# Performance work log

Measured on AMD Instinct MI355X. Metric: run time of the kernel, lower is better.

The kernel has to match this reference:

```python
import jax, jax.numpy as jnp
import numpy as np

N = 100000   # nodes
E = 1600000  # edges
NEG_SLOPE = 0.2
EPS = 1e-16


def _layer_norm(x, g, b):
    mu = jnp.mean(x, axis=-1, keepdims=True)
    var = jnp.mean((x - mu) ** 2, axis=-1, keepdims=True)
    return (x - mu) * jax.lax.rsqrt(var + 1e-5) * g + b


def _gat_layer(x, W, att_s, att_d, bias, src, dst, heads, C):
    n = x.shape[0]
    h = (x @ W.T).reshape(n, heads, C)            # [N,H,C]
    sa = jnp.sum(h * att_s, axis=-1)              # [N,H]
    da = jnp.sum(h * att_d, axis=-1)              # [N,H]
    logits = jax.nn.leaky_relu(sa[src] + da[dst], NEG_SLOPE)  # [E,H]
    m = jax.ops.segment_max(logits, dst, num_segments=n)      # [N,H]
    m = jnp.where(jnp.isfinite(m), m, 0.0)
    w = jnp.exp(logits - m[dst])                  # [E,H]
    denom = jax.ops.segment_sum(w, dst, num_segments=n)       # [N,H]
    msg = h[src] * w[:, :, None]                  # [E,H,C]
    agg = jax.ops.segment_sum(msg, dst, num_segments=n)       # [N,H,C]
    agg = agg / jnp.maximum(denom, EPS)[:, :, None]
    out = (agg + h).reshape(n, heads * C) + bias  # residual + bias
    return out


def setup_inputs() -> dict:
    key = jax.random.key(0)
    ks = jax.random.split(key, 16)
    s = 0.05
    inp = {
        "x": jax.random.normal(ks[0], (N, 128), jnp.float32),
        "edge_src": jax.random.randint(ks[1], (E,), 0, N, jnp.int32),
        "edge_dst": jax.random.randint(ks[2], (E,), 0, N, jnp.int32),
        # layer 1: in 128 -> heads=2, C=32 (out width 64)
        "W1": jax.random.normal(ks[3], (64, 128), jnp.float32) * s,
        "as1": jax.random.normal(ks[4], (2, 32), jnp.float32) * s,
        "ad1": jax.random.normal(ks[5], (2, 32), jnp.float32) * s,
        "b1": jnp.zeros((64,), jnp.float32),
        # layer 2: 64 -> heads=2, C=32
        "W2": jax.random.normal(ks[6], (64, 64), jnp.float32) * s,
        "as2": jax.random.normal(ks[7], (2, 32), jnp.float32) * s,
        "ad2": jax.random.normal(ks[8], (2, 32), jnp.float32) * s,
        "b2": jnp.zeros((64,), jnp.float32),
        # layer 3 (last): 64 -> heads=1, C=32
        "W3": jax.random.normal(ks[9], (32, 64), jnp.float32) * s,
        "as3": jax.random.normal(ks[10], (1, 32), jnp.float32) * s,
        "ad3": jax.random.normal(ks[11], (1, 32), jnp.float32) * s,
        "b3": jnp.zeros((32,), jnp.float32),
        "gamma1": jnp.ones((64,), jnp.float32),
        "beta1": jnp.zeros((64,), jnp.float32),
        "gamma2": jnp.ones((64,), jnp.float32),
        "beta2": jnp.zeros((64,), jnp.float32),
    }
    return inp


def reference(x, edge_src, edge_dst, W1, as1, ad1, b1, W2, as2, ad2, b2,
              W3, as3, ad3, b3, gamma1, beta1, gamma2, beta2):
    h = _gat_layer(x, W1, as1, ad1, b1, edge_src, edge_dst, 2, 32)
    h = jax.nn.relu(_layer_norm(h, gamma1, beta1))
    h = _gat_layer(h, W2, as2, ad2, b2, edge_src, edge_dst, 2, 32)
    h = jax.nn.relu(_layer_norm(h, gamma2, beta2))
    h = _gat_layer(h, W3, as3, ad3, b3, edge_src, edge_dst, 1, 32)
    return h
```

## Files before the change

### kernel.cpp

```cpp
#include <hip/hip_runtime.h>
#include <hip/hip_fp16.h>

#define LEAKY 0.2f
#define BSH 7
#define BN 128
#define CHUNK 4096
#define NBMAX 1024

__device__ __forceinline__ float leaky(float l) {
  return l >= 0.f ? l : LEAKY * l;
}

typedef _Float16 f16x2 __attribute__((ext_vector_type(2)));

__device__ __forceinline__ float fdot2(unsigned a, unsigned b, float c) {
#if __has_builtin(__builtin_amdgcn_fdot2)
  return __builtin_amdgcn_fdot2(__builtin_bit_cast(f16x2, a),
                                __builtin_bit_cast(f16x2, b), c, false);
#else
  __half2 ha = *(__half2*)&a, hb = *(__half2*)&b;
  float2 fa = __half22float2(ha), fb = __half22float2(hb);
  return fmaf(fa.x, fb.x, fmaf(fa.y, fb.y, c));
#endif
}

__device__ __forceinline__ int packsplat(float w) {
  const __half2 s = __half2half2(__float2half(w));
  return *(const int*)&s;
}
__device__ __forceinline__ __half2 asH2(unsigned u) { return *(__half2*)&u; }

template<int K, int CO, int H, bool IN_F32>
__global__ __launch_bounds__(256)
void gat_gemm4(const void* __restrict__ xin, const float* __restrict__ W,
               const float* __restrict__ atts, const float* __restrict__ attd,
               __half* __restrict__ hh, float* __restrict__ sa, float* __restrict__ da,
               int N) {
  constexpr int CG = CO / 4;
  constexpr int BM = (256 / CG) * 4;
  constexpr int C = CO / H;
  constexpr int LDW = K / 2 + 4;

  __shared__ unsigned xs[BM][LDW];
  __shared__ unsigned ws[CO][LDW];

  const int t = (int)threadIdx.x;
  const int cg = t % CG;
  const int ng = t / CG;
  const int n0 = (int)blockIdx.x * BM;

  if constexpr (IN_F32) {
    const float* x = (const float*)xin;
    constexpr int F4R = K / 4;
    constexpr int TOT = BM * F4R;
    for (int f = t; f < TOT; f += 256) {
      const int r = f / F4R, c4 = f % F4R;
      int row = n0 + r; row = row < N ? row : N - 1;
      const float4 v = *(const float4*)(x + (size_t)row * K + c4 * 4);
      const __half2 h0 = __floats2half2_rn(v.x, v.y);
      const __half2 h1 = __floats2half2_rn(v.z, v.w);
      xs[r][c4 * 2]     = *(const unsigned*)&h0;
      xs[r][c4 * 2 + 1] = *(const unsigned*)&h1;
    }
  } else {
    const __half* x = (const __half*)xin;
    constexpr int U4R = K / 8;
    constexpr int TOT = BM * U4R;
    for (int f = t; f < TOT; f += 256) {
      const int r = f / U4R, c = f % U4R;
      int row = n0 + r; row = row < N ? row : N - 1;
      const uint4 v = *(const uint4*)(x + (size_t)row * K + c * 8);
      *(uint4*)&xs[r][c * 4] = v;
    }
  }
  {
    constexpr int F4R = K / 4;
    constexpr int TOT = CO * F4R;
    for (int f = t; f < TOT; f += 256) {
      const int r = f / F4R, c4 = f % F4R;
      const float4 v = *(const float4*)(W + (size_t)r * K + c4 * 4);
      const __half2 h0 = __floats2half2_rn(v.x, v.y);
      const __half2 h1 = __floats2half2_rn(v.z, v.w);
      ws[r][c4 * 2]     = *(const unsigned*)&h0;
      ws[r][c4 * 2 + 1] = *(const unsigned*)&h1;
    }
  }
  __syncthreads();

  float acc[4][4] = {};
  #pragma unroll
  for (int k = 0; k < K; k += 8) {
    uint4 xa[4], wb[4];
    #pragma unroll
    for (int i = 0; i < 4; ++i) xa[i] = *(const uint4*)&xs[ng * 4 + i][k / 2];
    #pragma unroll
    for (int j = 0; j < 4; ++j) wb[j] = *(const uint4*)&ws[cg + CG * j][k / 2];
    #pragma unroll
    for (int i = 0; i < 4; ++i) {
      #pragma unroll
      for (int j = 0; j < 4; ++j) {
        acc[i][j] = fdot2(xa[i].x, wb[j].x, acc[i][j]);
        acc[i][j] = fdot2(xa[i].y, wb[j].y, acc[i][j]);
        acc[i][j] = fdot2(xa[i].z, wb[j].z, acc[i][j]);
        acc[i][j] = fdot2(xa[i].w, wb[j].w, acc[i][j]);
      }
    }
  }

  float as_[4], ad_[4];
  #pragma unroll
  for (int j = 0; j < 4; ++j) {
    as_[j] = atts[cg + CG * j];
    ad_[j] = attd[cg + CG * j];
  }
  float ps[4][H] = {}, pd[4][H] = {};
  #pragma unroll
  for (int i = 0; i < 4; ++i) {
    #pragma unroll
    for (int j = 0; j < 4; ++j) {
      const int hd = (CG * j) / C;
      ps[i][hd] = fmaf(acc[i][j], as_[j], ps[i][hd]);
      pd[i][hd] = fmaf(acc[i][j], ad_[j], pd[i][hd]);
    }
  }
  #pragma unroll
  for (int m = 1; m < CG; m <<= 1) {
    #pragma unroll
    for (int i = 0; i < 4; ++i) {
      #pragma unroll
      for (int hd = 0; hd < H; ++hd) {
        ps[i][hd] += __shfl_xor(ps[i][hd], m, 64);
        pd[i][hd] += __shfl_xor(pd[i][hd], m, 64);
      }
    }
  }

  #pragma unroll
  for (int i = 0; i < 4; ++i) {
    const int n = n0 + ng * 4 + i;
    if (n < N) {
      #pragma unroll
      for (int j = 0; j < 4; ++j)
        hh[(size_t)n * CO + cg + CG * j] = __float2half(acc[i][j]);
      if (cg == 0) {
        #pragma unroll
        for (int hd = 0; hd < H; ++hd) {
          sa[n * H + hd] = ps[i][hd];
          da[n * H + hd] = pd[i][hd];
        }
      }
    }
  }
}

__global__ __launch_bounds__(256)
void gat_edge2(const __half* __restrict__ hh,
               const float* __restrict__ sa, const float* __restrict__ da,
               const int* __restrict__ rowp, const int* __restrict__ col,
               const float* __restrict__ bias, const float* __restrict__ gamma,
               const float* __restrict__ beta, __half* __restrict__ out, int N) {
  __shared__ int2 wst[4][8][9][2];
  const int t = (int)threadIdx.x;
  const int lane = t & 63;
  const int wib = t >> 6;
  const int oct = lane >> 3;
  const int l = lane & 7;
  const int headq = l >> 2;
  const int wgl = (int)((blockIdx.x * blockDim.x + t) >> 6);
  const int n = wgl * 8 + oct;
  const bool valid = (n < N);
  const int nc = valid ? n : N - 1;
  const int beg = rowp[nc];
  const int end = rowp[nc + 1];
  const float2 dvv = *(const float2*)(da + (size_t)nc * 2);
  const __half* __restrict__ hp = hh;

  const __half2 z = __float2half2_rn(0.f);
  __half2 A0 = z, A1 = z, A2 = z, A3 = z;
  __half2 B0 = z, B1 = z, B2 = z, B3 = z;
  __half2 qA = z, qB = z;

  int sP = 0; float2 pP = make_float2(0.f, 0.f);
  if (beg < end) {
    const int c0 = min(8, end - beg);
    if (l < c0) { sP = col[beg + l]; pP = *(const float2*)(sa + (size_t)sP * 2); }
  }

  for (int b0 = beg; b0 < end; b0 += 8) {
    const int cnt = min(8, end - b0);
    if (l < cnt) {
      int2 e0; e0.x = sP; e0.y = packsplat(__expf(leaky(pP.x + dvv.x)));
      int2 e1; e1.x = sP; e1.y = packsplat(__expf(leaky(pP.y + dvv.y)));
      wst[wib][oct][l][0] = e0;
      wst[wib][oct][l][1] = e1;
    }
    const int nb0 = b0 + 8;
    if (nb0 < end) {
      const int ncnt = min(8, end - nb0);
      if (l < ncnt) { sP = col[nb0 + l]; pP = *(const float2*)(sa + (size_t)sP * 2); }
    }
    int i = 0;
    for (; i + 4 <= cnt; i += 4) {
      const int2 e0 = wst[wib][oct][i][headq];
      const int2 e1 = wst[wib][oct][i + 1][headq];
      const int2 e2 = wst[wib][oct][i + 2][headq];
      const int2 e3 = wst[wib][oct][i + 3][headq];
      const uint4 h0 = *(const uint4*)(hp + ((size_t)e0.x << 6) + 8 * l);
      const uint4 h1 = *(const uint4*)(hp + ((size_t)e1.x << 6) + 8 * l);
      const uint4 h2 = *(const uint4*)(hp + ((size_t)e2.x << 6) + 8 * l);
      const uint4 h3 = *(const uint4*)(hp + ((size_t)e3.x << 6) + 8 * l);
      const __half2 w0 = asH2(e0.y), w1 = asH2(e1.y), w2 = asH2(e2.y), w3 = asH2(e3.y);
      qA = __hadd2(qA, __hadd2(w0, w1));
      qB = __hadd2(qB, __hadd2(w2, w3));
      A0 = __hfma2(w0, asH2(h0.x), A0); A1 = __hfma2(w0, asH2(h0.y), A1);
      A2 = __hfma2(w0, asH2(h0.z), A2); A3 = __hfma2(w0, asH2(h0.w), A3);
      B0 = __hfma2(w1, asH2(h1.x), B0); B1 = __hfma2(w1, asH2(h1.y), B1);
      B2 = __hfma2(w1, asH2(h1.z), B2); B3 = __hfma2(w1, asH2(h1.w), B3);
      A0 = __hfma2(w2, asH2(h2.x), A0); A1 = __hfma2(w2, asH2(h2.y), A1);
      A2 = __hfma2(w2, asH2(h2.z), A2); A3 = __hfma2(w2, asH2(h2.w), A3);
      B0 = __hfma2(w3, asH2(h3.x), B0); B1 = __hfma2(w3, asH2(h3.y), B1);
      B2 = __hfma2(w3, asH2(h3.z), B2); B3 = __hfma2(w3, asH2(h3.w), B3);
    }
    for (; i < cnt; ++i) {
      const int2 e = wst[wib][oct][i][headq];
      const uint4 hv = *(const uint4*)(hp + ((size_t)e.x << 6) + 8 * l);
      const __half2 w = asH2(e.y);
      qA = __hadd2(qA, w);
      A0 = __hfma2(w, asH2(hv.x), A0); A1 = __hfma2(w, asH2(hv.y), A1);
      A2 = __hfma2(w, asH2(hv.z), A2); A3 = __hfma2(w, asH2(hv.w), A3);
    }
  }

  const float c0 = __low2float(A0) + __low2float(B0);
  const float c1 = __high2float(A0) + __high2float(B0);
  const float c2 = __low2float(A1) + __low2float(B1);
  const float c3 = __high2float(A1) + __high2float(B1);
  const float c4 = __low2float(A2) + __low2float(B2);
  const float c5 = __high2float(A2) + __high2float(B2);
  const float c6 = __low2float(A3) + __low2float(B3);
  const float c7 = __high2float(A3) + __high2float(B3);
  const float qf = __low2float(qA) + __low2float(qB);

  const float inv = 1.f / fmaxf(qf, 1e-16f);
  const uint4 hr = *(const uint4*)(hp + ((size_t)nc << 6) + 8 * l);
  const float2 r0 = __half22float2(asH2(hr.x));
  const float2 r1 = __half22float2(asH2(hr.y));
  const float2 r2 = __half22float2(asH2(hr.z));
  const float2 r3 = __half22float2(asH2(hr.w));
  const float4 bi0 = *(const float4*)(bias + 8 * l);
  const float4 bi1 = *(const float4*)(bias + 8 * l + 4);
  float v0 = c0 * inv + r0.x + bi0.x;
  float v1 = c1 * inv + r0.y + bi0.y;
  float v2 = c2 * inv + r1.x + bi0.z;
  float v3 = c3 * inv + r1.y + bi0.w;
  float v4 = c4 * inv + r2.x + bi1.x;
  float v5 = c5 * inv + r2.y + bi1.y;
  float v6 = c6 * inv + r3.x + bi1.z;
  float v7 = c7 * inv + r3.y + bi1.w;
  {
    float s = ((v0 + v1) + (v2 + v3)) + ((v4 + v5) + (v6 + v7));
    s += __shfl_xor(s, 1, 64); s += __shfl_xor(s, 2, 64); s += __shfl_xor(s, 4, 64);
    const float mu = s * (1.f / 64.f);
    const float d0 = v0 - mu, d1 = v1 - mu, d2 = v2 - mu, d3 = v3 - mu;
    const float d4 = v4 - mu, d5 = v5 - mu, d6 = v6 - mu, d7 = v7 - mu;
    float vs = ((d0 * d0 + d1 * d1) + (d2 * d2 + d3 * d3)) +
               ((d4 * d4 + d5 * d5) + (d6 * d6 + d7 * d7));
    vs += __shfl_xor(vs, 1, 64); vs += __shfl_xor(vs, 2, 64); vs += __shfl_xor(vs, 4, 64);
    const float rs = rsqrtf(vs * (1.f / 64.f) + 1e-5f);
    const float4 g0 = *(const float4*)(gamma + 8 * l);
    const float4 g1 = *(const float4*)(gamma + 8 * l + 4);
    const float4 e0 = *(const float4*)(beta + 8 * l);
    const float4 e1 = *(const float4*)(beta + 8 * l + 4);
    v0 = fmaxf(d0 * rs * g0.x + e0.x, 0.f);
    v1 = fmaxf(d1 * rs * g0.y + e0.y, 0.f);
    v2 = fmaxf(d2 * rs * g0.z + e0.z, 0.f);
    v3 = fmaxf(d3 * rs * g0.w + e0.w, 0.f);
    v4 = fmaxf(d4 * rs * g1.x + e1.x, 0.f);
    v5 = fmaxf(d5 * rs * g1.y + e1.y, 0.f);
    v6 = fmaxf(d6 * rs * g1.z + e1.z, 0.f);
    v7 = fmaxf(d7 * rs * g1.w + e1.w, 0.f);
  }
  if (valid) {
    const __half2 o0 = __floats2half2_rn(v0, v1);
    const __half2 o1 = __floats2half2_rn(v2, v3);
    const __half2 o2 = __floats2half2_rn(v4, v5);
    const __half2 o3 = __floats2half2_rn(v6, v7);
    uint4 o;
    o.x = *(const unsigned*)&o0; o.y = *(const unsigned*)&o1;
    o.z = *(const unsigned*)&o2; o.w = *(const unsigned*)&o3;
    *(uint4*)(out + (size_t)n * 64 + 8 * l) = o;
  }
}

__global__ __launch_bounds__(256)
void gat_edge1(const __half* __restrict__ hh,
               const float* __restrict__ sa, const float* __restrict__ da,
               const int* __restrict__ rowp, const int* __restrict__ col,
               const float* __restrict__ bias, float* __restrict__ out, int N) {
  __shared__ int2 wst[4][16][5];
  const int t = (int)threadIdx.x;
  const int lane = t & 63;
  const int wib = t >> 6;
  const int nq = lane >> 2;
  const int l = lane & 3;
  const int wgl = (int)((blockIdx.x * blockDim.x + t) >> 6);
  const int n = wgl * 16 + nq;
  const bool valid = (n < N);
  const int nc = valid ? n : N - 1;
  const int beg = rowp[nc];
  const int end = rowp[nc + 1];
  const float dv = da[nc];
  const __half* __restrict__ hp = hh;

  const __half2 z = __float2half2_rn(0.f);
  __half2 A0 = z, A1 = z, A2 = z, A3 = z;
  __half2 B0 = z, B1 = z, B2 = z, B3 = z;
  __half2 qA = z, qB = z;

  int sP = 0; float pP = 0.f;
  if (beg < end) {
    const int c0 = min(4, end - beg);
    if (l < c0) { sP = col[beg + l]; pP = sa[sP]; }
  }

  for (int b0 = beg; b0 < end; b0 += 4) {
    const int cnt = min(4, end - b0);
    if (l < cnt) {
      int2 e; e.x = sP; e.y = packsplat(__expf(leaky(pP + dv)));
      wst[wib][nq][l] = e;
    }
    const int nb0 = b0 + 4;
    if (nb0 < end) {
      const int ncnt = min(4, end - nb0);
      if (l < ncnt) { sP = col[nb0 + l]; pP = sa[sP]; }
    }
    if (cnt == 4) {
      const int2 e0 = wst[wib][nq][0];
      const int2 e1 = wst[wib][nq][1];
      const int2 e2 = wst[wib][nq][2];
      const int2 e3 = wst[wib][nq][3];
      const uint4 h0 = *(const uint4*)(hp + ((size_t)e0.x << 5) + 8 * l);
      const uint4 h1 = *(const uint4*)(hp + ((size_t)e1.x << 5) + 8 * l);
      const uint4 h2 = *(const uint4*)(hp + ((size_t)e2.x << 5) + 8 * l);
      const uint4 h3 = *(const uint4*)(hp + ((size_t)e3.x << 5) + 8 * l);
      const __half2 w0 = asH2(e0.y), w1 = asH2(e1.y), w2 = asH2(e2.y), w3 = asH2(e3.y);
      qA = __hadd2(qA, __hadd2(w0, w1));
      qB = __hadd2(qB, __hadd2(w2, w3));
      A0 = __hfma2(w0, asH2(h0.x), A0); A1 = __hfma2(w0, asH2(h0.y), A1);
      A2 = __hfma2(w0, asH2(h0.z), A2); A3 = __hfma2(w0, asH2(h0.w), A3);
      B0 = __hfma2(w1, asH2(h1.x), B0); B1 = __hfma2(w1, asH2(h1.y), B1);
      B2 = __hfma2(w1, asH2(h1.z), B2); B3 = __hfma2(w1, asH2(h1.w), B3);
      A0 = __hfma2(w2, asH2(h2.x), A0); A1 = __hfma2(w2, asH2(h2.y), A1);
      A2 = __hfma2(w2, asH2(h2.z), A2); A3 = __hfma2(w2, asH2(h2.w), A3);
      B0 = __hfma2(w3, asH2(h3.x), B0); B1 = __hfma2(w3, asH2(h3.y), B1);
      B2 = __hfma2(w3, asH2(h3.z), B2); B3 = __hfma2(w3, asH2(h3.w), B3);
    } else {
      for (int i = 0; i < cnt; ++i) {
        const int2 e = wst[wib][nq][i];
        const uint4 hv = *(const uint4*)(hp + ((size_t)e.x << 5) + 8 * l);
        const __half2 w = asH2(e.y);
        qA = __hadd2(qA, w);
        A0 = __hfma2(w, asH2(hv.x), A0); A1 = __hfma2(w, asH2(hv.y), A1);
        A2 = __hfma2(w, asH2(hv.z), A2); A3 = __hfma2(w, asH2(hv.w), A3);
      }
    }
  }

  if (valid) {
    const float c0 = __low2float(A0) + __low2float(B0);
    const float c1 = __high2float(A0) + __high2float(B0);
    const float c2 = __low2float(A1) + __low2float(B1);
    const float c3 = __high2float(A1) + __high2float(B1);
    const float c4 = __low2float(A2) + __low2float(B2);
    const float c5 = __high2float(A2) + __high2float(B2);
    const float c6 = __low2float(A3) + __low2float(B3);
    const float c7 = __high2float(A3) + __high2float(B3);
    const float qf = __low2float(qA) + __low2float(qB);
    const float inv = 1.f / fmaxf(qf, 1e-16f);
    const uint4 hr = *(const uint4*)(hp + ((size_t)nc << 5) + 8 * l);
    const float2 r0 = __half22float2(asH2(hr.x));
    const float2 r1 = __half22float2(asH2(hr.y));
    const float2 r2 = __half22float2(asH2(hr.z));
    const float2 r3 = __half22float2(asH2(hr.w));
    const float4 bi0 = *(const float4*)(bias + 8 * l);
    const float4 bi1 = *(const float4*)(bias + 8 * l + 4);
    float4 oA, oB;
    oA.x = c0 * inv + r0.x + bi0.x;
    oA.y = c1 * inv + r0.y + bi0.y;
    oA.z = c2 * inv + r1.x + bi0.z;
    oA.w = c3 * inv + r1.y + bi0.w;
    oB.x = c4 * inv + r2.x + bi1.x;
    oB.y = c5 * inv + r2.y + bi1.y;
    oB.z = c6 * inv + r3.x + bi1.z;
    oB.w = c7 * inv + r3.y + bi1.w;
    *(float4*)(out + (size_t)n * 32 + 8 * l) = oA;
    *(float4*)(out + (size_t)n * 32 + 8 * l + 4) = oB;
  }
}

__global__ __launch_bounds__(256)
void k_hist_chunk(const int* __restrict__ dst, int* __restrict__ cntmat,
                  int E, int NB, int NW) {
  __shared__ int lh[NBMAX];
  const int t = (int)threadIdx.x;
  const int chunk = (int)blockIdx.x;
  const int c0 = chunk * CHUNK;
  const int cnt = min(CHUNK, E - c0);
  for (int b = t; b < NB; b += 256) lh[b] = 0;
  __syncthreads();
  for (int i = t; i < cnt; i += 256)
    atomicAdd(&lh[dst[c0 + i] >> BSH], 1);
  __syncthreads();
  for (int b = t; b < NB; b += 256)
    cntmat[(size_t)b * NW + chunk] = lh[b];
}

template<int VPT>
__global__ __launch_bounds__(256)
void k_colscan(int* __restrict__ cntmat, int* __restrict__ bcnt, int NW) {
  __shared__ int sm[256];
  const int b = (int)blockIdx.x;
  int* row = cntmat + (size_t)b * NW;
  const int t = (int)threadIdx.x;
  int v[VPT];
  int run = 0;
  #pragma unroll
  for (int j = 0; j < VPT; ++j) {
    const int c = t * VPT + j;
    v[j] = (c < NW) ? row[c] : 0;
    run += v[j];
  }
  sm[t] = run;
  __syncthreads();
  #pragma unroll
  for (int off = 1; off < 256; off <<= 1) {
    int xv = (t >= off) ? sm[t - off] : 0;
    __syncthreads();
    sm[t] += xv;
    __syncthreads();
  }
  int excl = sm[t] - run;
  #pragma unroll
  for (int j = 0; j < VPT; ++j) {
    const int c = t * VPT + j;
    if (c < NW) row[c] = excl;
    excl += v[j];
  }
  if (t == 255) bcnt[b] = sm[255];
}

__global__ void k_bscan(const int* __restrict__ bcnt, int nb,
                        int* __restrict__ bstart, int* __restrict__ rowp_last, int E) {
  __shared__ int sm[256];
  const int t = (int)threadIdx.x;
  int v[4];
  #pragma unroll
  for (int j = 0; j < 4; ++j) { int i = t * 4 + j; v[j] = (i < nb) ? bcnt[i] : 0; }
  const int tot = v[0] + v[1] + v[2] + v[3];
  sm[t] = tot; __syncthreads();
  #pragma unroll
  for (int off = 1; off < 256; off <<= 1) {
    int xv = (t >= off) ? sm[t - off] : 0;
    __syncthreads();
    sm[t] += xv;
    __syncthreads();
  }
  int excl = sm[t] - tot;
  #pragma unroll
  for (int j = 0; j < 4; ++j) {
    int i = t * 4 + j;
    if (i < nb) { bstart[i] = excl; excl += v[j]; }
  }
  if (t == 0) { bstart[nb] = E; *rowp_last = E; }
}

__global__ __launch_bounds__(256)
void k_part(const int* __restrict__ src, const int* __restrict__ dst,
            const int* __restrict__ bstart, const int* __restrict__ cntmat,
            int* __restrict__ pairs, int E, int NB, int NW) {
  __shared__ int lh[NBMAX];
  __shared__ int lofs[NBMAX];
  __shared__ int gofs[NBMAX];
  __shared__ int stg[CHUNK];
  __shared__ short stgb[CHUNK];
  __shared__ int bsum[256];
  const int t = (int)threadIdx.x;
  const int chunk = (int)blockIdx.x;
  const int c0 = chunk * CHUNK;
  const int cnt = min(CHUNK, E - c0);

  for (int b = t; b < NB; b += 256) lh[b] = 0;
  __syncthreads();
  for (int i = t; i < cnt; i += 256)
    atomicAdd(&lh[dst[c0 + i] >> BSH], 1);
  __syncthreads();

  int v[4]; int run = 0;
  #pragma unroll
  for (int j = 0; j < 4; ++j) {
    const int b = t * 4 + j;
    v[j] = (b < NB) ? lh[b] : 0;
    run += v[j];
  }
  bsum[t] = run;
  __syncthreads();
  #pragma unroll
  for (int off = 1; off < 256; off <<= 1) {
    int xv = (t >= off) ? bsum[t - off] : 0;
    __syncthreads();
    bsum[t] += xv;
    __syncthreads();
  }
  int base = bsum[t] - run;
  #pragma unroll
  for (int j = 0; j < 4; ++j) {
    const int b = t * 4 + j;
    if (b < NB) lofs[b] = base;
    base += v[j];
  }
  __syncthreads();

  for (int b = t; b < NB; b += 256) {
    gofs[b] = bstart[b] + cntmat[(size_t)b * NW + chunk];
    lh[b] = lofs[b];
  }
  __syncthreads();

  for (int i = t; i < cnt; i += 256) {
    const int d = dst[c0 + i];
    const int b = d >> BSH;
    const int p = atomicAdd(&lh[b], 1);
    stg[p] = (src[c0 + i] << BSH) | (d & (BN - 1));
    stgb[p] = (short)b;
  }
  __syncthreads();

  for (int i = t; i < cnt; i += 256) {
    const int b = (int)stgb[i];
    pairs[gofs[b] + (i - lofs[b])] = stg[i];
  }
}

__global__ __launch_bounds__(256)
void k_bucket_csr(const int* __restrict__ pairs, const int* __restrict__ bstart,
                  int* __restrict__ rowp, int* __restrict__ col, int N) {
  __shared__ int ldeg[BN];
  __shared__ int lofs[BN];
  const int b = (int)blockIdx.x;
  const int t = (int)threadIdx.x;
  const int base = b << BSH;
  const int nn = min(BN, N - base);
  const int s0 = bstart[b];
  const int s1 = bstart[b + 1];

  if (t < BN) ldeg[t] = 0;
  __syncthreads();
  for (int i = s0 + t; i < s1; i += 256)
    atomicAdd(&ldeg[pairs[i] & (BN - 1)], 1);
  __syncthreads();
  if (t < BN) lofs[t] = ldeg[t];
  __syncthreads();
  #pragma unroll
  for (int off = 1; off < BN; off <<= 1) {
    int v = (t < BN && t >= off) ? lofs[t - off] : 0;
    __syncthreads();
    if (t < BN) lofs[t] += v;
    __syncthreads();
  }
  if (t < BN) {
    const int ofs = s0 + lofs[t] - ldeg[t];
    if (t < nn) rowp[base + t] = ofs;
    ldeg[t] = ofs;
  }
  __syncthreads();
  for (int i = s0 + t; i < s1; i += 256) {
    const int pr = pairs[i];
    const int p = atomicAdd(&ldeg[pr & (BN - 1)], 1);
    col[p] = pr >> BSH;
  }
}

extern "C" void kernel_launch(void* const* d_in, const int* in_sizes, int n_in,
                              void* d_out, int out_size, void* d_ws, size_t ws_size,
                              hipStream_t stream) {
  const float* x   = (const float*)d_in[0];
  const int* esrc  = (const int*)d_in[1];
  const int* edst  = (const int*)d_in[2];
  const float* W1  = (const float*)d_in[3];
  const float* as1 = (const float*)d_in[4];
  const float* ad1 = (const float*)d_in[5];
  const float* b1  = (const float*)d_in[6];
  const float* W2  = (const float*)d_in[7];
  const float* as2 = (const float*)d_in[8];
  const float* ad2 = (const float*)d_in[9];
  const float* b2  = (const float*)d_in[10];
  const float* W3  = (const float*)d_in[11];
  const float* as3 = (const float*)d_in[12];
  const float* ad3 = (const float*)d_in[13];
  const float* b3  = (const float*)d_in[14];
  const float* g1  = (const float*)d_in[15];
  const float* be1 = (const float*)d_in[16];
  const float* g2  = (const float*)d_in[17];
  const float* be2 = (const float*)d_in[18];

  const int N = in_sizes[0] / 128;
  const int E = in_sizes[1];
  const int NB = (N + BN - 1) / BN;
  const int NW = (E + CHUNK - 1) / CHUNK;

  char* ws = (char*)d_ws;
  size_t off = 0;
  auto alloc = [&](size_t bytes) -> void* {
    void* p = ws + off;
    off = (off + bytes + 255) & ~(size_t)255;
    return p;
  };
  __half* lnbuf = (__half*)alloc((size_t)N * 64 * 2);
  __half* hh   = (__half*)alloc((size_t)N * 64 * 2);
  float* sab   = (float*)alloc((size_t)N * 2 * 4);
  float* dab   = (float*)alloc((size_t)N * 2 * 4);
  int* rowp    = (int*)alloc((size_t)(N + 1) * 4);
  int* colb    = (int*)alloc((size_t)E * 4);
  int* bcnt    = (int*)alloc((size_t)NB * 4);
  int* bstart  = (int*)alloc((size_t)(NB + 1) * 4);
  int* cntmat  = (int*)alloc((size_t)NB * NW * 4);
  int* pairs = (E <= out_size) ? (int*)d_out : (int*)alloc((size_t)E * 4);
  (void)ws_size; (void)n_in;

  k_hist_chunk<<<NW, 256, 0, stream>>>(edst, cntmat, E, NB, NW);
  if (NW <= 512)        k_colscan<2><<<NB, 256, 0, stream>>>(cntmat, bcnt, NW);
  else if (NW <= 1024)  k_colscan<4><<<NB, 256, 0, stream>>>(cntmat, bcnt, NW);
  else                  k_colscan<8><<<NB, 256, 0, stream>>>(cntmat, bcnt, NW);
  k_bscan<<<1, 256, 0, stream>>>(bcnt, NB, bstart, rowp + N, E);
  k_part<<<NW, 256, 0, stream>>>(esrc, edst, bstart, cntmat, pairs, E, NB, NW);
  k_bucket_csr<<<NB, 256, 0, stream>>>(pairs, bstart, rowp, colb, N);

  const int gG12 = (N + 63) / 64;
  const int gG3  = (N + 127) / 128;
  const int gE2 = (N + 31) / 32;
  const int gE1 = (N + 63) / 64;

  gat_gemm4<128, 64, 2, true><<<gG12, 256, 0, stream>>>(x, W1, as1, ad1, hh, sab, dab, N);
  gat_edge2<<<gE2, 256, 0, stream>>>(hh, sab, dab, rowp, colb, b1, g1, be1, lnbuf, N);

  gat_gemm4<64, 64, 2, false><<<gG12, 256, 0, stream>>>(lnbuf, W2, as2, ad2, hh, sab, dab, N);
  gat_edge2<<<gE2, 256, 0, stream>>>(hh, sab, dab, rowp, colb, b2, g2, be2, lnbuf, N);

  gat_gemm4<64, 32, 1, false><<<gG3, 256, 0, stream>>>(lnbuf, W3, as3, ad3, hh, sab, dab, N);
  gat_edge1<<<gE1, 256, 0, stream>>>(hh, sab, dab, rowp, colb, b3, (float*)d_out, N);
}
```

Baseline: 216.8 us.

## Replace fdot2 SIMT GEMM with MFMA 16x16x32 f16 matrix-core GEMM

The node projection GEMM now runs on MFMA 16x16x32 f16 matrix instructions instead of scalar fdot2 accumulation. A fragments are loaded from global memory straight into registers, and only W is staged in LDS. Each wave computes a 16-row tile across all output columns, and the attention dot products are reduced with 16-lane shuffles. This cuts the ALU and LDS cost of the GEMM stage. In exchange it adds uncoalesced per-lane row loads and the edge kernels are left unchanged, so the effect on the total is limited by the GEMM's share of runtime.

```diff
diff --git a/kernel.cpp b/kernel.cpp
--- a/kernel.cpp
+++ b/kernel.cpp
@@ -11,18 +11,8 @@
   return l >= 0.f ? l : LEAKY * l;
 }
 
-typedef _Float16 f16x2 __attribute__((ext_vector_type(2)));
-
-__device__ __forceinline__ float fdot2(unsigned a, unsigned b, float c) {
-#if __has_builtin(__builtin_amdgcn_fdot2)
-  return __builtin_amdgcn_fdot2(__builtin_bit_cast(f16x2, a),
-                                __builtin_bit_cast(f16x2, b), c, false);
-#else
-  __half2 ha = *(__half2*)&a, hb = *(__half2*)&b;
-  float2 fa = __half22float2(ha), fb = __half22float2(hb);
-  return fmaf(fa.x, fb.x, fmaf(fa.y, fb.y, c));
-#endif
-}
+typedef _Float16 f16x8 __attribute__((ext_vector_type(8)));
+typedef float f32x4 __attribute__((ext_vector_type(4)));
 
 __device__ __forceinline__ int packsplat(float w) {
   const __half2 s = __half2half2(__float2half(w));
@@ -32,121 +22,109 @@
 
 template<int K, int CO, int H, bool IN_F32>
 __global__ __launch_bounds__(256)
-void gat_gemm4(const void* __restrict__ xin, const float* __restrict__ W,
+void gat_gemm5(const void* __restrict__ xin, const float* __restrict__ W,
                const float* __restrict__ atts, const float* __restrict__ attd,
                __half* __restrict__ hh, float* __restrict__ sa, float* __restrict__ da,
                int N) {
-  constexpr int CG = CO / 4;
-  constexpr int BM = (256 / CG) * 4;
+  constexpr int NT = CO / 16;
+  constexpr int KB = K / 32;
+  constexpr int LDH = K + 8;
   constexpr int C = CO / H;
-  constexpr int LDW = K / 2 + 4;
-
-  __shared__ unsigned xs[BM][LDW];
-  __shared__ unsigned ws[CO][LDW];
-
-  const int t = (int)threadIdx.x;
-  const int cg = t % CG;
-  const int ng = t / CG;
-  const int n0 = (int)blockIdx.x * BM;
-
+
+  __shared__ __half wsh[CO][LDH];
+
+  const int t = (int)threadIdx.x;
+  const int lane = t & 63;
+  const int w = t >> 6;
+  const int n0 = (int)blockIdx.x * 64;
+  const int l15 = lane & 15;
+  const int kofs = (lane >> 4) * 8;
+
+  for (int f = t; f < CO * K / 4; f += 256) {
+    const int r = f / (K / 4), c4 = f % (K / 4);
+    const float4 v = *(const float4*)(W + (size_t)r * K + c4 * 4);
+    *(__half2*)&wsh[r][c4 * 4]     = __floats2half2_rn(v.x, v.y);
+    *(__half2*)&wsh[r][c4 * 4 + 2] = __floats2half2_rn(v.z, v.w);
+  }
+
+  int arow = n0 + 16 * w + l15;
+  arow = arow < N ? arow : N - 1;
+  f16x8 afr[KB];
   if constexpr (IN_F32) {
     const float* x = (const float*)xin;
-    constexpr int F4R = K / 4;
-    constexpr int TOT = BM * F4R;
-    for (int f = t; f < TOT; f += 256) {
-      const int r = f / F4R, c4 = f % F4R;
-      int row = n0 + r; row = row < N ? row : N - 1;
-      const float4 v = *(const float4*)(x + (size_t)row * K + c4 * 4);
-      const __half2 h0 = __floats2half2_rn(v.x, v.y);
-      const __half2 h1 = __floats2half2_rn(v.z, v.w);
-      xs[r][c4 * 2]     = *(const unsigned*)&h0;
-      xs[r][c4 * 2 + 1] = *(const unsigned*)&h1;
+    #pragma unroll
+    for (int kb = 0; kb < KB; ++kb) {
+      const float* p = x + (size_t)arow * K + kb * 32 + kofs;
+      const float4 u = *(const float4*)p;
+      const float4 v = *(const float4*)(p + 4);
+      union { f16x8 f; __half2 h[4]; } U;
+      U.h[0] = __floats2half2_rn(u.x, u.y);
+      U.h[1] = __floats2half2_rn(u.z, u.w);
+      U.h[2] = __floats2half2_rn(v.x, v.y);
+      U.h[3] = __floats2half2_rn(v.z, v.w);
+      afr[kb] = U.f;
     }
   } else {
     const __half* x = (const __half*)xin;
-    constexpr int U4R = K / 8;
-    constexpr int TOT = BM * U4R;
-    for (int f = t; f < TOT; f += 256) {
-      const int r = f / U4R, c = f % U4R;
-      int row = n0 + r; row = row < N ? row : N - 1;
-      const uint4 v = *(const uint4*)(x + (size_t)row * K + c * 8);
-      *(uint4*)&xs[r][c * 4] = v;
-    }
-  }
-  {
-    constexpr int F4R = K / 4;
-    constexpr int TOT = CO * F4R;
-    for (int f = t; f < TOT; f += 256) {
-      const int r = f / F4R, c4 = f % F4R;
-      const float4 v = *(const float4*)(W + (size_t)r * K + c4 * 4);
-      const __half2 h0 = __floats2half2_rn(v.x, v.y);
-      const __half2 h1 = __floats2half2_rn(v.z, v.w);
-      ws[r][c4 * 2]     = *(const unsigned*)&h0;
-      ws[r][c4 * 2 + 1] = *(const unsigned*)&h1;
-    }
-  }
-  __syncthreads();
-
-  float acc[4][4] = {};
-  #pragma unroll
-  for (int k = 0; k < K; k += 8) {
-    uint4 xa[4], wb[4];
     #pragma unroll
-    for (int i = 0; i < 4; ++i) xa[i] = *(const uint4*)&xs[ng * 4 + i][k / 2];
+    for (int kb = 0; kb < KB; ++kb)
+      afr[kb] = *(const f16x8*)(x + (size_t)arow * K + kb * 32 + kofs);
+  }
+  __syncthreads();
+
+  f32x4 acc[NT];
+  #pragma unroll
+  for (int tt = 0; tt < NT; ++tt) { f32x4 zf = {0.f, 0.f, 0.f, 0.f}; acc[tt] = zf; }
+  #pragma unroll
+  for (int kb = 0; kb < KB; ++kb) {
     #pragma unroll
-    for (int j = 0; j < 4; ++j) wb[j] = *(const uint4*)&ws[cg + CG * j][k / 2];
+    for (int tt = 0; tt < NT; ++tt) {
+      const f16x8 bfr = *(const f16x8*)&wsh[16 * tt + l15][kb * 32 + kofs];
+      acc[tt] = __builtin_amdgcn_mfma_f32_16x16x32_f16(afr[kb], bfr, acc[tt], 0, 0, 0);
+    }
+  }
+
+  float as_[NT], ad_[NT];
+  #pragma unroll
+  for (int tt = 0; tt < NT; ++tt) {
+    as_[tt] = atts[16 * tt + l15];
+    ad_[tt] = attd[16 * tt + l15];
+  }
+  float ps[4][H] = {}, pd[4][H] = {};
+  #pragma unroll
+  for (int tt = 0; tt < NT; ++tt) {
+    const int hd = (16 * tt) / C;
     #pragma unroll
-    for (int i = 0; i < 4; ++i) {
-      #pragma unroll
-      for (int j = 0; j < 4; ++j) {
-        acc[i][j] = fdot2(xa[i].x, wb[j].x, acc[i][j]);
-        acc[i][j] = fdot2(xa[i].y, wb[j].y, acc[i][j]);
-        acc[i][j] = fdot2(xa[i].z, wb[j].z, acc[i][j]);
-        acc[i][j] = fdot2(xa[i].w, wb[j].w, acc[i][j]);
-      }
-    }
-  }
-
-  float as_[4], ad_[4];
-  #pragma unroll
-  for (int j = 0; j < 4; ++j) {
-    as_[j] = atts[cg + CG * j];
-    ad_[j] = attd[cg + CG * j];
-  }
-  float ps[4][H] = {}, pd[4][H] = {};
-  #pragma unroll
-  for (int i = 0; i < 4; ++i) {
+    for (int r = 0; r < 4; ++r) {
+      ps[r][hd] = fmaf(acc[tt][r], as_[tt], ps[r][hd]);
+      pd[r][hd] = fmaf(acc[tt][r], ad_[tt], pd[r][hd]);
+    }
+  }
+  #pragma unroll
+  for (int m = 1; m < 16; m <<= 1) {
     #pragma unroll
-    for (int j = 0; j < 4; ++j) {
-      const int hd = (CG * j) / C;
-      ps[i][hd] = fmaf(acc[i][j], as_[j], ps[i][hd]);
-      pd[i][hd] = fmaf(acc[i][j], ad_[j], pd[i][hd]);
-    }
-  }
-  #pragma unroll
-  for (int m = 1; m < CG; m <<= 1) {
-    #pragma unroll
-    for (int i = 0; i < 4; ++i) {
+    for (int r = 0; r < 4; ++r) {
       #pragma unroll
       for (int hd = 0; hd < H; ++hd) {
-        ps[i][hd] += __shfl_xor(ps[i][hd], m, 64);
-        pd[i][hd] += __shfl_xor(pd[i][hd], m, 64);
+        ps[r][hd] += __shfl_xor(ps[r][hd], m, 64);
+        pd[r][hd] += __shfl_xor(pd[r][hd], m, 64);
       }
     }
   }
 
-  #pragma unroll
-  for (int i = 0; i < 4; ++i) {
-    const int n = n0 + ng * 4 + i;
-    if (n < N) {
+  const int obase = n0 + 16 * w + ((lane >> 4) << 2);
+  #pragma unroll
+  for (int r = 0; r < 4; ++r) {
+    const int node = obase + r;
+    if (node < N) {
       #pragma unroll
-      for (int j = 0; j < 4; ++j)
-        hh[(size_t)n * CO + cg + CG * j] = __float2half(acc[i][j]);
-      if (cg == 0) {
+      for (int tt = 0; tt < NT; ++tt)
+        hh[(size_t)node * CO + 16 * tt + l15] = __float2half(acc[tt][r]);
+      if (l15 == 0) {
         #pragma unroll
         for (int hd = 0; hd < H; ++hd) {
-          sa[n * H + hd] = ps[i][hd];
-          da[n * H + hd] = pd[i][hd];
+          sa[node * H + hd] = ps[r][hd];
+          da[node * H + hd] = pd[r][hd];
         }
       }
     }
@@ -635,17 +613,16 @@
   k_part<<<NW, 256, 0, stream>>>(esrc, edst, bstart, cntmat, pairs, E, NB, NW);
   k_bucket_csr<<<NB, 256, 0, stream>>>(pairs, bstart, rowp, colb, N);
 
-  const int gG12 = (N + 63) / 64;
-  const int gG3  = (N + 127) / 128;
+  const int gG  = (N + 63) / 64;
   const int gE2 = (N + 31) / 32;
   const int gE1 = (N + 63) / 64;
 
-  gat_gemm4<128, 64, 2, true><<<gG12, 256, 0, stream>>>(x, W1, as1, ad1, hh, sab, dab, N);
+  gat_gemm5<128, 64, 2, true><<<gG, 256, 0, stream>>>(x, W1, as1, ad1, hh, sab, dab, N);
   gat_edge2<<<gE2, 256, 0, stream>>>(hh, sab, dab, rowp, colb, b1, g1, be1, lnbuf, N);
 
-  gat_gemm4<64, 64, 2, false><<<gG12, 256, 0, stream>>>(lnbuf, W2, as2, ad2, hh, sab, dab, N);
+  gat_gemm5<64, 64, 2, false><<<gG, 256, 0, stream>>>(lnbuf, W2, as2, ad2, hh, sab, dab, N);
   gat_edge2<<<gE2, 256, 0, stream>>>(hh, sab, dab, rowp, colb, b2, g2, be2, lnbuf, N);
 
-  gat_gemm4<64, 32, 1, false><<<gG3, 256, 0, stream>>>(lnbuf, W3, as3, ad3, hh, sab, dab, N);
+  gat_gemm5<64, 32, 1, false><<<gG, 256, 0, stream>>>(lnbuf, W3, as3, ad3, hh, sab, dab, N);
   gat_edge1<<<gE1, 256, 0, stream>>>(hh, sab, dab, rowp, colb, b3, (float*)d_out, N);
 }
```

New measurement: 196.8 us, median of 4. -9.2%, faster.
